# Optimization experiments

Hardware: AMD Instinct MI355X
Metric: run time of the kernel (lower is better)

The kernel has to match this reference:

```python
import jax, jax.numpy as jnp
import numpy as np

N_NODES = 50000
N_EDGES = 800000
IN_C, HID_C, OUT_C = 256, 512, 256
DROP_P = 0.5


def _glorot(key, fan_in, fan_out):
    lim = float(np.sqrt(6.0 / (fan_in + fan_out)))
    return jax.random.uniform(key, (fan_in, fan_out), jnp.float32, -lim, lim)


def setup_inputs() -> dict:
    key = jax.random.key(0)
    k_x, k_e, k_w1, k_w2 = jax.random.split(key, 4)
    tensor = jax.random.normal(k_x, (N_NODES, IN_C), dtype=jnp.float32)
    edge_index = jax.random.randint(k_e, (2, N_EDGES), 0, N_NODES, dtype=jnp.int64)
    W1 = _glorot(k_w1, IN_C, HID_C)
    b1 = jnp.zeros((HID_C,), jnp.float32)
    W2 = _glorot(k_w2, HID_C, OUT_C)
    b2 = jnp.zeros((OUT_C,), jnp.float32)
    return {"tensor": tensor, "edge_index": edge_index,
            "W1": W1, "b1": b1, "W2": W2, "b2": b2}


def _gcn_conv(x, W, b, row, col, n_nodes):
    # PyG GCNConv: x' = D^-1/2 (A + I) D^-1/2 (x W) + b
    x = x @ W                                            # [N, F_out]
    # degree over targets including self-loops
    deg = jax.ops.segment_sum(jnp.ones_like(col, dtype=x.dtype), col,
                              num_segments=n_nodes) + 1.0
    dinv = jnp.where(deg > 0, jax.lax.rsqrt(deg), 0.0)   # [N]
    norm = dinv[row] * dinv[col]                         # [E]
    msg = x[row] * norm[:, None]                         # [E, F_out] gather
    out = jax.ops.segment_sum(msg, col, num_segments=n_nodes)  # scatter-add
    out = out + x * (dinv * dinv)[:, None]               # self-loop term
    return out + b


def _dropout(x, key, p=DROP_P):
    keep = jax.random.bernoulli(key, 1.0 - p, x.shape)
    return jnp.where(keep, x / (1.0 - p), 0.0)


def reference(tensor, edge_index, W1, b1, W2, b2):
    row, col = edge_index[0], edge_index[1]
    k1, k2 = jax.random.split(jax.random.key(42))
    x = _gcn_conv(tensor, W1, b1, row, col, N_NODES)
    x = _dropout(jax.nn.relu(x), k1)
    x = _gcn_conv(x, W2, b2, row, col, N_NODES)
    x = _dropout(jax.nn.relu(x), k2)
    return x
```

## Files before the change

### kernel.cpp

```cpp
#include <hip/hip_runtime.h>
#include <stdint.h>


#define N_NODES 50000
#define N_EDGES 800000
#define M_PAD   50048
#define IN_C 256
#define HID_C 512
#define OUT_C 256

typedef __attribute__((ext_vector_type(8))) short bf16x8;
typedef __attribute__((ext_vector_type(4))) float f32x4;

struct U2 { unsigned a, b; };

__host__ __device__ constexpr unsigned rotl32(unsigned x, int d) {
  return (x << d) | (x >> (32 - d));
}

#define TF_ROUND(r) { x0 += x1; x1 = rotl32(x1, (r)); x1 ^= x0; }

__host__ __device__ constexpr U2 threefry2x32(unsigned k0, unsigned k1,
                                              unsigned x0, unsigned x1) {
  unsigned ks2 = k0 ^ k1 ^ 0x1BD11BDAu;
  x0 += k0; x1 += k1;
  TF_ROUND(13) TF_ROUND(15) TF_ROUND(26) TF_ROUND(6)  x0 += k1;  x1 += ks2 + 1u;
  TF_ROUND(17) TF_ROUND(29) TF_ROUND(16) TF_ROUND(24) x0 += ks2; x1 += k0 + 2u;
  TF_ROUND(13) TF_ROUND(15) TF_ROUND(26) TF_ROUND(6)  x0 += k0;  x1 += k1 + 3u;
  TF_ROUND(17) TF_ROUND(29) TF_ROUND(16) TF_ROUND(24) x0 += k1;  x1 += ks2 + 4u;
  TF_ROUND(13) TF_ROUND(15) TF_ROUND(26) TF_ROUND(6)  x0 += ks2; x1 += k0 + 5u;
  return U2{x0, x1};
}

__device__ __forceinline__ float drop_apply(float v, unsigned idx, unsigned k0, unsigned k1) {
  v = fmaxf(v, 0.f);
  U2 r = threefry2x32(k0, k1, 0u, idx);
  unsigned bits = r.a ^ r.b;
  return (bits >> 31) ? 0.f : v * 2.0f;
}

__device__ __forceinline__ ushort f2b(float f) {
  unsigned u = __builtin_bit_cast(unsigned, f);
  unsigned r = (u + 0x7fffu + ((u >> 16) & 1u)) >> 16;
  return (ushort)r;
}
__device__ __forceinline__ float b2f_hi(unsigned u) {
  return __builtin_bit_cast(float, u & 0xffff0000u);
}
__device__ __forceinline__ float b2f_lo(unsigned u) {
  return __builtin_bit_cast(float, u << 16);
}

__device__ __forceinline__ void acc8(float (&a)[8], uint4 u, float wgt) {
  a[0] += b2f_lo(u.x) * wgt; a[1] += b2f_hi(u.x) * wgt;
  a[2] += b2f_lo(u.y) * wgt; a[3] += b2f_hi(u.y) * wgt;
  a[4] += b2f_lo(u.z) * wgt; a[5] += b2f_hi(u.z) * wgt;
  a[6] += b2f_lo(u.w) * wgt; a[7] += b2f_hi(u.w) * wgt;
}

__device__ __forceinline__ void gload16(const void* g, void* l) {
  __builtin_amdgcn_global_load_lds(
      (const __attribute__((address_space(1))) void*)g,
      (__attribute__((address_space(3))) void*)l, 16, 0, 0);
}

__global__ void deg_kernel(const int* __restrict__ col, int* __restrict__ cnt, int E) {
  int e = blockIdx.x * 256 + threadIdx.x;
  if (e < E) atomicAdd(&cnt[col[e]], 1);
}

__global__ void dinv_kernel(const int* __restrict__ cnt, float* __restrict__ dinv, int N) {
  int n = blockIdx.x * 256 + threadIdx.x;
  if (n < N) dinv[n] = rsqrtf((float)cnt[n] + 1.0f);
}

__global__ __launch_bounds__(1024) void scan_local(const int* __restrict__ cnt,
                                                   int* __restrict__ indptr,
                                                   int* __restrict__ chunkSums, int n) {
  __shared__ int s[1024];
  int gid = blockIdx.x * 1024 + threadIdx.x;
  int v = (gid < n) ? cnt[gid] : 0;
  s[threadIdx.x] = v;
  __syncthreads();
#pragma unroll
  for (int off = 1; off < 1024; off <<= 1) {
    int t = (threadIdx.x >= off) ? s[threadIdx.x - off] : 0;
    __syncthreads();
    s[threadIdx.x] += t;
    __syncthreads();
  }
  if (gid < n) indptr[gid] = s[threadIdx.x] - v;
  if (threadIdx.x == 1023) chunkSums[blockIdx.x] = s[1023];
}

__global__ void scan_chunks(int* __restrict__ chunkSums, int nChunks) {
  if (threadIdx.x == 0 && blockIdx.x == 0) {
    int acc = 0;
    for (int i = 0; i < nChunks; ++i) { int t = chunkSums[i]; chunkSums[i] = acc; acc += t; }
  }
}

__global__ void add_offsets(int* __restrict__ indptr, const int* __restrict__ chunkSums,
                            int n, int total) {
  int gid = blockIdx.x * 256 + threadIdx.x;
  if (gid < n) indptr[gid] += chunkSums[gid >> 10];
  if (gid == 0) indptr[n] = total;
}

__global__ void build_csr(const int* __restrict__ row, const int* __restrict__ col,
                          const int* __restrict__ indptr, int* __restrict__ cursor,
                          const float* __restrict__ dinv,
                          int2* __restrict__ srcW, int E) {
  int e = blockIdx.x * 256 + threadIdx.x;
  if (e < E) {
    int r = row[e];
    int c = col[e];
    int p = indptr[c] + atomicAdd(&cursor[c], 1);
    srcW[p] = make_int2(r, __builtin_bit_cast(int, dinv[r]));
  }
}

__global__ void cvt_f32_bf16(const float* __restrict__ in, ushort* __restrict__ out, int n4) {
  int i = blockIdx.x * 256 + threadIdx.x;
  if (i < n4) {
    float4 v = *(const float4*)(in + (size_t)i * 4);
    ushort4 o = make_ushort4(f2b(v.x), f2b(v.y), f2b(v.z), f2b(v.w));
    *(ushort4*)(out + (size_t)i * 4) = o;
  }
}

template <int LOGK>
__global__ void wT_kernel(const float* __restrict__ W, ushort* __restrict__ WT, int N, int total) {
  int i = blockIdx.x * 256 + threadIdx.x;
  if (i < total) {
    int k = i & ((1 << LOGK) - 1);
    int n = i >> LOGK;
    WT[i] = f2b(W[(size_t)k * N + n]);
  }
}

template <bool EPI>
__global__ __launch_bounds__(256) void gather_pair(const ushort* __restrict__ X,
                                                   const int* __restrict__ indptr,
                                                   const int2* __restrict__ srcW,
                                                   const float* __restrict__ dinv,
                                                   const float* __restrict__ bias,
                                                   void* __restrict__ outp,
                                                   const unsigned char* __restrict__ mask2,
                                                   int N) {
  int wid = (blockIdx.x * 256 + threadIdx.x) >> 6;
  int lane = threadIdx.x & 63;
  if (wid >= N) return;
  const int sub = lane >> 5;
  const int fi = lane & 31;
  const int f0 = fi * 8;
  int beg = __builtin_amdgcn_readfirstlane(indptr[wid]);
  int end = __builtin_amdgcn_readfirstlane(indptr[wid + 1]);
  float dc = dinv[wid];

  float a[8] = {};
  if (sub == 0) {
    uint4 u = *(const uint4*)(X + (size_t)wid * 256 + f0);
    acc8(a, u, dc);
  }
  int eb = beg;
  for (; eb + 8 <= end; eb += 8) {
    int2 q0 = srcW[eb + 0 + sub];
    int2 q1 = srcW[eb + 2 + sub];
    int2 q2 = srcW[eb + 4 + sub];
    int2 q3 = srcW[eb + 6 + sub];
    uint4 u0 = *(const uint4*)(X + (size_t)q0.x * 256 + f0);
    uint4 u1 = *(const uint4*)(X + (size_t)q1.x * 256 + f0);
    uint4 u2 = *(const uint4*)(X + (size_t)q2.x * 256 + f0);
    uint4 u3 = *(const uint4*)(X + (size_t)q3.x * 256 + f0);
    acc8(a, u0, __builtin_bit_cast(float, q0.y));
    acc8(a, u1, __builtin_bit_cast(float, q1.y));
    acc8(a, u2, __builtin_bit_cast(float, q2.y));
    acc8(a, u3, __builtin_bit_cast(float, q3.y));
  }
  for (int e = eb + sub; e < end; e += 2) {
    int2 q = srcW[e];
    uint4 u = *(const uint4*)(X + (size_t)q.x * 256 + f0);
    acc8(a, u, __builtin_bit_cast(float, q.y));
  }
#pragma unroll
  for (int j = 0; j < 8; ++j) {
    a[j] += __shfl_xor(a[j], 32);
    a[j] *= dc;
  }

  if (EPI) {
    float4 bv0 = *(const float4*)(bias + f0);
    float4 bv1 = *(const float4*)(bias + f0 + 4);
    unsigned mk = mask2[(size_t)wid * 32 + fi];
    float v[8];
    v[0] = fmaxf(a[0] + bv0.x, 0.f); v[1] = fmaxf(a[1] + bv0.y, 0.f);
    v[2] = fmaxf(a[2] + bv0.z, 0.f); v[3] = fmaxf(a[3] + bv0.w, 0.f);
    v[4] = fmaxf(a[4] + bv1.x, 0.f); v[5] = fmaxf(a[5] + bv1.y, 0.f);
    v[6] = fmaxf(a[6] + bv1.z, 0.f); v[7] = fmaxf(a[7] + bv1.w, 0.f);
#pragma unroll
    for (int j = 0; j < 8; ++j) v[j] = ((mk >> j) & 1u) ? 0.f : v[j] * 2.0f;
    float4 o;
    if (sub == 0) o = make_float4(v[0], v[1], v[2], v[3]);
    else          o = make_float4(v[4], v[5], v[6], v[7]);
    *(float4*)((float*)outp + (size_t)wid * 256 + f0 + sub * 4) = o;
  } else {
    uint2 o;
    if (sub == 0) {
      o.x = (unsigned)f2b(a[0]) | ((unsigned)f2b(a[1]) << 16);
      o.y = (unsigned)f2b(a[2]) | ((unsigned)f2b(a[3]) << 16);
    } else {
      o.x = (unsigned)f2b(a[4]) | ((unsigned)f2b(a[5]) << 16);
      o.y = (unsigned)f2b(a[6]) | ((unsigned)f2b(a[7]) << 16);
    }
    *(uint2*)((ushort*)outp + (size_t)wid * 256 + f0 + sub * 4) = o;
  }
}

template <int MODE>
__global__ __launch_bounds__(256) void gemm_bf16(const ushort* __restrict__ A,
                                                 const ushort* __restrict__ BT,
                                                 ushort* __restrict__ C,
                                                 int M, int K, int N,
                                                 const float* __restrict__ bias,
                                                 unsigned char* __restrict__ maskOut,
                                                 unsigned kk0, unsigned kk1) {
  __shared__ __align__(16) ushort lds[4 * 128 * 64];
  const int tid = threadIdx.x;
  const int lane = tid & 63;
  const int wv = tid >> 6;
  const int wr = wv >> 1, wc = wv & 1;
  const int bm = blockIdx.x * 128;
  const int bn = blockIdx.y * 128;

  f32x4 acc[4][4] = {};
  const int xorv = (lane & 7) << 4;

  auto stage = [&](int buf, int k0) {
#pragma unroll
    for (int l = 0; l < 4; ++l) {
      int cid = l * 256 + tid;
      int row = cid >> 3;
      int kcol = ((cid & 7) ^ (row & 7)) * 8;
      gload16(A + (size_t)(bm + row) * K + k0 + kcol, (void*)(lds + buf * 8192 + cid * 8));
      gload16(BT + (size_t)(bn + row) * K + k0 + kcol, (void*)(lds + (2 + buf) * 8192 + cid * 8));
    }
  };

  const int nt = K >> 6;
  stage(0, 0);
  __syncthreads();
  int cur = 0;
  for (int t = 0; t < nt; ++t) {
    if (t + 1 < nt) stage(cur ^ 1, (t + 1) << 6);
    const char* Ab = (const char*)(lds + cur * 8192);
    const char* Bb = (const char*)(lds + (2 + cur) * 8192);
#pragma unroll
    for (int ks = 0; ks < 2; ++ks) {
      bf16x8 af[4], bf[4];
      const int kb = (ks * 64 + (lane >> 4) * 16) ^ xorv;
#pragma unroll
      for (int i = 0; i < 4; ++i) {
        int arow = wr * 64 + i * 16 + (lane & 15);
        af[i] = *(const bf16x8*)(Ab + arow * 128 + kb);
        int brow = wc * 64 + i * 16 + (lane & 15);
        bf[i] = *(const bf16x8*)(Bb + brow * 128 + kb);
      }
#pragma unroll
      for (int m = 0; m < 4; ++m)
#pragma unroll
        for (int n = 0; n < 4; ++n)
          acc[m][n] = __builtin_amdgcn_mfma_f32_16x16x32_bf16(af[m], bf[n], acc[m][n], 0, 0, 0);
    }
    __syncthreads();
    cur ^= 1;
  }

  ushort* Csm = (ushort*)lds;
  const int rowoff = wr * 64 + ((lane >> 4) << 2);
  const int coloff = wc * 64 + (lane & 15);
  float bias_v[4];
  if (MODE == 1) {
#pragma unroll
    for (int n = 0; n < 4; ++n) bias_v[n] = bias[bn + coloff + n * 16];
  }
#pragma unroll
  for (int m = 0; m < 4; ++m) {
#pragma unroll
    for (int r = 0; r < 4; ++r) {
      int lrow = rowoff + m * 16 + r;
#pragma unroll
      for (int n = 0; n < 4; ++n) {
        float v = acc[m][n][r];
        if (MODE == 1) {
          unsigned idx = (unsigned)(bm + lrow) * (unsigned)N + (unsigned)(bn + coloff + n * 16);
          v = drop_apply(v + bias_v[n], idx, kk0, kk1);
        }
        Csm[lrow * 132 + coloff + n * 16] = f2b(v);
      }
    }
  }
  __syncthreads();
  {
    int row = tid >> 1, ch = (tid & 1) * 64;
    const ushort* src = Csm + row * 132 + ch;
    ushort* dst = C + (size_t)(bm + row) * N + bn + ch;
#pragma unroll
    for (int j = 0; j < 8; ++j)
      *(bf16x8*)(dst + j * 8) = *(const bf16x8*)(src + j * 8);
    if (MODE == 2) {
      int grow = bm + row;
      unsigned base = (unsigned)grow * (unsigned)N + (unsigned)(bn + ch);
      unsigned long long mword = 0;
#pragma unroll
      for (int j = 0; j < 64; ++j) {
        U2 rr = threefry2x32(kk0, kk1, 0u, base + (unsigned)j);
        mword |= (unsigned long long)(((rr.a ^ rr.b) >> 31) & 1u) << j;
      }
      *(unsigned long long*)(maskOut + (size_t)(base >> 3)) = mword;
    }
  }
}

extern "C" void kernel_launch(void* const* d_in, const int* in_sizes, int n_in,
                              void* d_out, int out_size, void* d_ws, size_t ws_size,
                              hipStream_t stream) {
  const float* x  = (const float*)d_in[0];
  const int*   ei = (const int*)d_in[1];
  const float* W1 = (const float*)d_in[2];
  const float* b1 = (const float*)d_in[3];
  const float* W2 = (const float*)d_in[4];
  const float* b2 = (const float*)d_in[5];
  float* out = (float*)d_out;
  (void)in_sizes; (void)n_in; (void)out_size; (void)ws_size;

  const int* row = ei;
  const int* col = ei + N_EDGES;

  char* ws = (char*)d_ws;
  float*  dinv      = (float*) (ws);
  int*    cnt       = (int*)   (ws + (1u << 18));
  int*    indptr    = (int*)   (ws + (2u << 18));
  int*    cursor    = (int*)   (ws + (3u << 18));
  int*    chunkSums = (int*)   (ws + (1u << 20));
  int2*   srcW      = (int2*)  (ws + 2u * (1u << 20));
  ushort* W1T       = (ushort*)(ws + 9u * (1u << 20));
  ushort* W2T       = (ushort*)(ws + 9u * (1u << 20) + (1u << 19));
  unsigned char* mask2 = (unsigned char*)(ws + 10u * (1u << 20));
  ushort* x16       = (ushort*)(ws + 14u * (1u << 20));
  ushort* aggB      = (ushort*)(ws + 40u * (1u << 20));
  ushort* h         = (ushort*)(ws + 66u * (1u << 20));
  ushort* hw2       = (ushort*)(ws + 118u* (1u << 20));

  constexpr U2 K1 = threefry2x32(0u, 42u, 0u, 0u);
  constexpr U2 K2 = threefry2x32(0u, 42u, 0u, 1u);

  (void)hipMemsetAsync(cnt, 0, N_NODES * sizeof(int), stream);
  (void)hipMemsetAsync(cursor, 0, N_NODES * sizeof(int), stream);
  deg_kernel<<<(N_EDGES + 255) / 256, 256, 0, stream>>>(col, cnt, N_EDGES);
  dinv_kernel<<<(N_NODES + 255) / 256, 256, 0, stream>>>(cnt, dinv, N_NODES);
  const int nChunks = (N_NODES + 1023) / 1024;
  scan_local<<<nChunks, 1024, 0, stream>>>(cnt, indptr, chunkSums, N_NODES);
  scan_chunks<<<1, 64, 0, stream>>>(chunkSums, nChunks);
  add_offsets<<<(N_NODES + 255) / 256, 256, 0, stream>>>(indptr, chunkSums, N_NODES, N_EDGES);
  build_csr<<<(N_EDGES + 255) / 256, 256, 0, stream>>>(row, col, indptr, cursor, dinv, srcW, N_EDGES);

  cvt_f32_bf16<<<(N_NODES * IN_C / 4 + 255) / 256, 256, 0, stream>>>(x, x16, N_NODES * IN_C / 4);
  wT_kernel<8><<<(IN_C * HID_C + 255) / 256, 256, 0, stream>>>(W1, W1T, HID_C, IN_C * HID_C);
  wT_kernel<9><<<(HID_C * OUT_C + 255) / 256, 256, 0, stream>>>(W2, W2T, OUT_C, HID_C * OUT_C);
  (void)hipMemsetAsync(aggB + (size_t)N_NODES * IN_C, 0, (size_t)(M_PAD - N_NODES) * IN_C * 2, stream);

  gather_pair<false><<<(N_NODES + 3) / 4, 256, 0, stream>>>(
      x16, indptr, srcW, dinv, nullptr, aggB, nullptr, N_NODES);
  gemm_bf16<1><<<dim3(M_PAD / 128, HID_C / 128), 256, 0, stream>>>(
      aggB, W1T, h, M_PAD, IN_C, HID_C, b1, nullptr, K1.a, K1.b);

  gemm_bf16<2><<<dim3(M_PAD / 128, OUT_C / 128), 256, 0, stream>>>(
      h, W2T, hw2, M_PAD, HID_C, OUT_C, nullptr, mask2, K2.a, K2.b);
  gather_pair<true><<<(N_NODES + 3) / 4, 256, 0, stream>>>(
      hw2, indptr, srcW, dinv, b2, out, mask2, N_NODES);
}
```

Baseline: 375.1 us.

## Gather full rows per wave with 16-deep edge unroll; single-buffer GEMM LDS

Result: no change. 370.1 us (-1.3%).

```diff
diff --git a/kernel.cpp b/kernel.cpp
--- a/kernel.cpp
+++ b/kernel.cpp
@@ -51,11 +51,9 @@
   return __builtin_bit_cast(float, u << 16);
 }
 
-__device__ __forceinline__ void acc8(float (&a)[8], uint4 u, float wgt) {
+__device__ __forceinline__ void acc4(float (&a)[4], uint2 u, float wgt) {
   a[0] += b2f_lo(u.x) * wgt; a[1] += b2f_hi(u.x) * wgt;
   a[2] += b2f_lo(u.y) * wgt; a[3] += b2f_hi(u.y) * wgt;
-  a[4] += b2f_lo(u.z) * wgt; a[5] += b2f_hi(u.z) * wgt;
-  a[6] += b2f_lo(u.w) * wgt; a[7] += b2f_hi(u.w) * wgt;
 }
 
 __device__ __forceinline__ void gload16(const void* g, void* l) {
@@ -140,7 +138,7 @@
 }
 
 template <bool EPI>
-__global__ __launch_bounds__(256) void gather_pair(const ushort* __restrict__ X,
+__global__ __launch_bounds__(256, 4) void gather16(const ushort* __restrict__ X,
                                                    const int* __restrict__ indptr,
                                                    const int2* __restrict__ srcW,
                                                    const float* __restrict__ dinv,
@@ -151,69 +149,67 @@
   int wid = (blockIdx.x * 256 + threadIdx.x) >> 6;
   int lane = threadIdx.x & 63;
   if (wid >= N) return;
-  const int sub = lane >> 5;
-  const int fi = lane & 31;
-  const int f0 = fi * 8;
+  const int f0 = lane * 4;
   int beg = __builtin_amdgcn_readfirstlane(indptr[wid]);
   int end = __builtin_amdgcn_readfirstlane(indptr[wid + 1]);
   float dc = dinv[wid];
 
-  float a[8] = {};
-  if (sub == 0) {
-    uint4 u = *(const uint4*)(X + (size_t)wid * 256 + f0);
-    acc8(a, u, dc);
-  }
-  int eb = beg;
-  for (; eb + 8 <= end; eb += 8) {
-    int2 q0 = srcW[eb + 0 + sub];
-    int2 q1 = srcW[eb + 2 + sub];
-    int2 q2 = srcW[eb + 4 + sub];
-    int2 q3 = srcW[eb + 6 + sub];
-    uint4 u0 = *(const uint4*)(X + (size_t)q0.x * 256 + f0);
-    uint4 u1 = *(const uint4*)(X + (size_t)q1.x * 256 + f0);
-    uint4 u2 = *(const uint4*)(X + (size_t)q2.x * 256 + f0);
-    uint4 u3 = *(const uint4*)(X + (size_t)q3.x * 256 + f0);
-    acc8(a, u0, __builtin_bit_cast(float, q0.y));
-    acc8(a, u1, __builtin_bit_cast(float, q1.y));
-    acc8(a, u2, __builtin_bit_cast(float, q2.y));
-    acc8(a, u3, __builtin_bit_cast(float, q3.y));
-  }
-  for (int e = eb + sub; e < end; e += 2) {
+  float a[4] = {};
+  {
+    uint2 u = *(const uint2*)(X + (size_t)wid * 256 + f0);
+    acc4(a, u, dc);
+  }
+  int e = beg;
+  for (; e + 16 <= end; e += 16) {
+    int2 q[16];
+#pragma unroll
+    for (int j = 0; j < 16; ++j) q[j] = srcW[e + j];
+    uint2 u[16];
+#pragma unroll
+    for (int j = 0; j < 16; ++j)
+      u[j] = *(const uint2*)(X + (size_t)q[j].x * 256 + f0);
+#pragma unroll
+    for (int j = 0; j < 16; ++j)
+      acc4(a, u[j], __builtin_bit_cast(float, q[j].y));
+  }
+  for (; e + 4 <= end; e += 4) {
+    int2 q[4];
+#pragma unroll
+    for (int j = 0; j < 4; ++j) q[j] = srcW[e + j];
+    uint2 u[4];
+#pragma unroll
+    for (int j = 0; j < 4; ++j)
+      u[j] = *(const uint2*)(X + (size_t)q[j].x * 256 + f0);
+#pragma unroll
+    for (int j = 0; j < 4; ++j)
+      acc4(a, u[j], __builtin_bit_cast(float, q[j].y));
+  }
+  for (; e < end; ++e) {
     int2 q = srcW[e];
-    uint4 u = *(const uint4*)(X + (size_t)q.x * 256 + f0);
-    acc8(a, u, __builtin_bit_cast(float, q.y));
-  }
-#pragma unroll
-  for (int j = 0; j < 8; ++j) {
-    a[j] += __shfl_xor(a[j], 32);
-    a[j] *= dc;
-  }
+    uint2 u = *(const uint2*)(X + (size_t)q.x * 256 + f0);
+    acc4(a, u, __builtin_bit_cast(float, q.y));
+  }
+#pragma unroll
+  for (int j = 0; j < 4; ++j) a[j] *= dc;
 
   if (EPI) {
-    float4 bv0 = *(const float4*)(bias + f0);
-    float4 bv1 = *(const float4*)(bias + f0 + 4);
-    unsigned mk = mask2[(size_t)wid * 32 + fi];
-    float v[8];
-    v[0] = fmaxf(a[0] + bv0.x, 0.f); v[1] = fmaxf(a[1] + bv0.y, 0.f);
-    v[2] = fmaxf(a[2] + bv0.z, 0.f); v[3] = fmaxf(a[3] + bv0.w, 0.f);
-    v[4] = fmaxf(a[4] + bv1.x, 0.f); v[5] = fmaxf(a[5] + bv1.y, 0.f);
-    v[6] = fmaxf(a[6] + bv1.z, 0.f); v[7] = fmaxf(a[7] + bv1.w, 0.f);
-#pragma unroll
-    for (int j = 0; j < 8; ++j) v[j] = ((mk >> j) & 1u) ? 0.f : v[j] * 2.0f;
-    float4 o;
-    if (sub == 0) o = make_float4(v[0], v[1], v[2], v[3]);
-    else          o = make_float4(v[4], v[5], v[6], v[7]);
-    *(float4*)((float*)outp + (size_t)wid * 256 + f0 + sub * 4) = o;
+    float4 bv = *(const float4*)(bias + f0);
+    unsigned mk = mask2[(size_t)wid * 32 + (lane >> 1)];
+    int sh = (lane & 1) * 4;
+    float v0 = fmaxf(a[0] + bv.x, 0.f);
+    float v1 = fmaxf(a[1] + bv.y, 0.f);
+    float v2 = fmaxf(a[2] + bv.z, 0.f);
+    float v3 = fmaxf(a[3] + bv.w, 0.f);
+    v0 = ((mk >> (sh + 0)) & 1u) ? 0.f : v0 * 2.0f;
+    v1 = ((mk >> (sh + 1)) & 1u) ? 0.f : v1 * 2.0f;
+    v2 = ((mk >> (sh + 2)) & 1u) ? 0.f : v2 * 2.0f;
+    v3 = ((mk >> (sh + 3)) & 1u) ? 0.f : v3 * 2.0f;
+    *(float4*)((float*)outp + (size_t)wid * 256 + f0) = make_float4(v0, v1, v2, v3);
   } else {
     uint2 o;
-    if (sub == 0) {
-      o.x = (unsigned)f2b(a[0]) | ((unsigned)f2b(a[1]) << 16);
-      o.y = (unsigned)f2b(a[2]) | ((unsigned)f2b(a[3]) << 16);
-    } else {
-      o.x = (unsigned)f2b(a[4]) | ((unsigned)f2b(a[5]) << 16);
-      o.y = (unsigned)f2b(a[6]) | ((unsigned)f2b(a[7]) << 16);
-    }
-    *(uint2*)((ushort*)outp + (size_t)wid * 256 + f0 + sub * 4) = o;
+    o.x = (unsigned)f2b(a[0]) | ((unsigned)f2b(a[1]) << 16);
+    o.y = (unsigned)f2b(a[2]) | ((unsigned)f2b(a[3]) << 16);
+    *(uint2*)((ushort*)outp + (size_t)wid * 256 + f0) = o;
   }
 }
 
@@ -225,7 +221,7 @@
                                                  const float* __restrict__ bias,
                                                  unsigned char* __restrict__ maskOut,
                                                  unsigned kk0, unsigned kk1) {
-  __shared__ __align__(16) ushort lds[4 * 128 * 64];
+  __shared__ __align__(16) ushort lds[16896];
   const int tid = threadIdx.x;
   const int lane = tid & 63;
   const int wv = tid >> 6;
@@ -236,25 +232,20 @@
   f32x4 acc[4][4] = {};
   const int xorv = (lane & 7) << 4;
 
-  auto stage = [&](int buf, int k0) {
+  const int nt = K >> 6;
+  for (int t = 0; t < nt; ++t) {
+    const int k0 = t << 6;
 #pragma unroll
     for (int l = 0; l < 4; ++l) {
       int cid = l * 256 + tid;
       int row = cid >> 3;
       int kcol = ((cid & 7) ^ (row & 7)) * 8;
-      gload16(A + (size_t)(bm + row) * K + k0 + kcol, (void*)(lds + buf * 8192 + cid * 8));
-      gload16(BT + (size_t)(bn + row) * K + k0 + kcol, (void*)(lds + (2 + buf) * 8192 + cid * 8));
+      gload16(A + (size_t)(bm + row) * K + k0 + kcol, (void*)(lds + cid * 8));
+      gload16(BT + (size_t)(bn + row) * K + k0 + kcol, (void*)(lds + 8192 + cid * 8));
     }
-  };
-
-  const int nt = K >> 6;
-  stage(0, 0);
-  __syncthreads();
-  int cur = 0;
-  for (int t = 0; t < nt; ++t) {
-    if (t + 1 < nt) stage(cur ^ 1, (t + 1) << 6);
-    const char* Ab = (const char*)(lds + cur * 8192);
-    const char* Bb = (const char*)(lds + (2 + cur) * 8192);
+    __syncthreads();
+    const char* Ab = (const char*)lds;
+    const char* Bb = (const char*)(lds + 8192);
 #pragma unroll
     for (int ks = 0; ks < 2; ++ks) {
       bf16x8 af[4], bf[4];
@@ -273,7 +264,6 @@
           acc[m][n] = __builtin_amdgcn_mfma_f32_16x16x32_bf16(af[m], bf[n], acc[m][n], 0, 0, 0);
     }
     __syncthreads();
-    cur ^= 1;
   }
 
   ushort* Csm = (ushort*)lds;
@@ -370,13 +360,13 @@
   wT_kernel<9><<<(HID_C * OUT_C + 255) / 256, 256, 0, stream>>>(W2, W2T, OUT_C, HID_C * OUT_C);
   (void)hipMemsetAsync(aggB + (size_t)N_NODES * IN_C, 0, (size_t)(M_PAD - N_NODES) * IN_C * 2, stream);
 
-  gather_pair<false><<<(N_NODES + 3) / 4, 256, 0, stream>>>(
+  gather16<false><<<(N_NODES + 3) / 4, 256, 0, stream>>>(
       x16, indptr, srcW, dinv, nullptr, aggB, nullptr, N_NODES);
   gemm_bf16<1><<<dim3(M_PAD / 128, HID_C / 128), 256, 0, stream>>>(
       aggB, W1T, h, M_PAD, IN_C, HID_C, b1, nullptr, K1.a, K1.b);
 
   gemm_bf16<2><<<dim3(M_PAD / 128, OUT_C / 128), 256, 0, stream>>>(
       h, W2T, hw2, M_PAD, HID_C, OUT_C, nullptr, mask2, K2.a, K2.b);
-  gather_pair<true><<<(N_NODES + 3) / 4, 256, 0, stream>>>(
+  gather16<true><<<(N_NODES + 3) / 4, 256, 0, stream>>>(
       hw2, indptr, srcW, dinv, b2, out, mask2, N_NODES);
 }
```
